# Performance work log

Measured on AMD Instinct MI355X. Metric: run time of the kernel, lower is better.

Reference implementation:

```python
import jax, jax.numpy as jnp
import numpy as np

N, F, H, K_SUB, DEPTH = 500_000, 64, 32, 16, 4
N_NODES = 2 ** DEPTH - 1   # 15 internal nodes
N_LEAVES = 2 ** DEPTH      # 16 leaves
SLOPE = 0.01               # torch LeakyReLU default negative_slope


def _leaky(v):
    return jnp.where(v >= 0, v, SLOPE * v)


def setup_inputs() -> dict:
    key = jax.random.key(0)
    ks = jax.random.split(key, 8)
    x = jax.random.normal(ks[0], (N, F), dtype=jnp.float32)
    subset_idx = jax.random.randint(ks[1], (N_NODES, K_SUB), 0, F, dtype=jnp.int32)
    W1 = jax.random.normal(ks[2], (N_NODES, H, K_SUB), dtype=jnp.float32) * (1.0 / np.sqrt(K_SUB))
    b1 = jnp.zeros((N_NODES, H), jnp.float32)
    W2 = jax.random.normal(ks[3], (N_NODES, H, H), dtype=jnp.float32) * (1.0 / np.sqrt(H))
    b2 = jnp.zeros((N_NODES, H), jnp.float32)
    W3 = jax.random.normal(ks[4], (N_NODES, 2, H), dtype=jnp.float32) * (1.0 / np.sqrt(H))
    b3 = jnp.zeros((N_NODES, 2), jnp.float32)
    # leaf 'best' constants (class modes precomputed by populate_best)
    leaf_best = jax.random.randint(ks[5], (N_LEAVES,), 0, 10).astype(jnp.float32)
    return {"x": x, "W1": W1, "b1": b1, "W2": W2, "b2": b2, "W3": W3, "b3": b3,
            "leaf_best": leaf_best, "subset_idx": subset_idx}


def _forward(x, W1, b1, W2, b2, W3, b3, leaf_best, subset_idx):
    n = x.shape[0]
    loc = jnp.zeros((n,), jnp.int32)   # local node index within current level
    off = 0
    for level in range(DEPTH):
        k = 2 ** level
        sl = slice(off, off + k)
        xs = x[:, subset_idx[sl]]                                   # [N, k, K_SUB]
        h = _leaky(jnp.einsum('nkf,khf->nkh', xs, W1[sl]) + b1[sl])  # [N, k, H]
        h = _leaky(jnp.einsum('nkh,kgh->nkg', h, W2[sl]) + b2[sl])   # [N, k, H]
        logits = jnp.einsum('nkh,koh->nko', h, W3[sl]) + b3[sl]      # [N, k, 2]
        p0 = jax.nn.softmax(logits, axis=-1)[..., 0]                 # [N, k]
        p0_row = jnp.take_along_axis(p0, loc[:, None], axis=1)[:, 0]
        bit = (p0_row < 0.5).astype(jnp.int32)  # 0 -> left, 1 -> right
        loc = 2 * loc + bit
        off += k
    return leaf_best[loc]  # [N]


def reference(x, W1, b1, W2, b2, W3, b3, leaf_best, subset_idx):
    return _forward(x, W1, b1, W2, b2, W3, b3, leaf_best, subset_idx)
```

## Files before the change

kernel.cpp:

```cpp
#include <hip/hip_runtime.h>

#define NF 64
#define NH 32
#define NK 16
#define NNODES 15
#define BLOCK 512
#define NWAVES (BLOCK / 64)


__global__ __attribute__((amdgpu_flat_work_group_size(BLOCK, BLOCK),
                          amdgpu_waves_per_eu(2, 4)))
void tree_mlp_kernel(
    const float* __restrict__ x,
    const float* __restrict__ W1, const float* __restrict__ b1,
    const float* __restrict__ W2, const float* __restrict__ b2,
    const float* __restrict__ W3, const float* __restrict__ b3,
    const float* __restrict__ leaf_best, const int* __restrict__ subset_idx,
    float* __restrict__ out, int N)
{
    __shared__ __align__(16) float W2Lv[8 * 1024];
    __shared__ int      subL[NNODES * NK];
    __shared__ unsigned permL[BLOCK];
    __shared__ int      sortL[64];

    const int tid  = threadIdx.x;
    const int lane = tid & 63;
    const int wv   = tid >> 6;

    for (int i = tid; i < NNODES * NK; i += BLOCK) subL[i] = subset_idx[i];
    {
        const float4* src = (const float4*)W2;
        float4* dst = (float4*)W2Lv;
        for (int i = tid; i < 256; i += BLOCK) dst[i] = src[i];
    }
    __syncthreads();

    const int s = blockIdx.x * BLOCK + tid;
    int valid = (s < N) ? 1 : 0;
    int id    = valid ? s : 0;
    int loc = 0, off = 0;

    #pragma unroll 1
    for (int level = 0; level < 4; ++level) {
        if (level > 0) {
            const int nb = 1 << level;
            int myrank = 0;
            #pragma unroll 1
            for (int b = 0; b < nb; ++b) {
                const unsigned long long m = __ballot(loc == b);
                if (loc == b)
                    myrank = __popcll(m & ((1ull << lane) - 1ull));
                if (lane == 0)
                    sortL[b * NWAVES + wv] = __popcll(m);
            }
            __syncthreads();

            {
                const int cnt4 = (1 << level) * 256;
                const float4* src = (const float4*)(W2 + (size_t)off * 1024);
                float4* dst = (float4*)W2Lv;
                for (int i = tid; i < cnt4; i += BLOCK) dst[i] = src[i];
            }
            if (wv == 0) {
                const int cnt = nb * NWAVES;
                int v = (lane < cnt) ? sortL[lane] : 0;
                int incl = v;
                #pragma unroll
                for (int d = 1; d < 64; d <<= 1) {
                    int t = __shfl_up(incl, d, 64);
                    if (lane >= d) incl += t;
                }
                if (lane < cnt) sortL[lane] = incl - v;
            }
            __syncthreads();

            const int slot = sortL[loc * NWAVES + wv] + myrank;
            permL[slot] = ((unsigned)id << 5) | ((unsigned)valid << 4) | (unsigned)loc;
            __syncthreads();
            const unsigned p = permL[tid];
            id    = (int)(p >> 5);
            valid = (int)((p >> 4) & 1u);
            loc   = (int)(p & 15u);
            __syncthreads();
        }

        const int node = off + loc;
        const float* xr = x + (size_t)id * NF;

        float xs[NK];
        const int* si = subL + node * NK;
        #pragma unroll
        for (int k = 0; k < NK; ++k) xs[k] = xr[si[k]];

        float h1v[NH];
        {
            const float4* w1g = (const float4*)(W1 + node * (NH * NK));
            const float*  b1g = b1 + node * NH;
            #pragma unroll
            for (int j = 0; j < NH; ++j) {
                float acc = b1g[j];
                #pragma unroll
                for (int q = 0; q < NK / 4; ++q) {
                    const float4 t = w1g[j * 4 + q];
                    acc += t.x * xs[q * 4 + 0];
                    acc += t.y * xs[q * 4 + 1];
                    acc += t.z * xs[q * 4 + 2];
                    acc += t.w * xs[q * 4 + 3];
                }
                h1v[j] = (acc >= 0.f) ? acc : 0.01f * acc;
            }
        }

        const float* w2l = W2Lv + (loc << 10);
        const float* bb2 = b2 + node * NH;
        const float* w3g = W3 + node * 2 * NH;
        float l0 = b3[node * 2 + 0];
        float l1 = b3[node * 2 + 1];

        #pragma unroll 2
        for (int g = 0; g < NH; ++g) {
            float acc = bb2[g];
            const float4* row = (const float4*)(w2l + g * NH);
            #pragma unroll
            for (int q = 0; q < NH / 4; ++q) {
                const float4 t = row[q];
                acc += t.x * h1v[q * 4 + 0];
                acc += t.y * h1v[q * 4 + 1];
                acc += t.z * h1v[q * 4 + 2];
                acc += t.w * h1v[q * 4 + 3];
            }
            const float h2 = (acc >= 0.f) ? acc : 0.01f * acc;
            l0 += w3g[g]      * h2;
            l1 += w3g[NH + g] * h2;
        }

        const int bit = (l0 < l1) ? 1 : 0;
        loc = 2 * loc + bit;
        off = 2 * off + 1;
    }

    if (valid) out[id] = leaf_best[loc];
}

extern "C" void kernel_launch(void* const* d_in, const int* in_sizes, int n_in,
                              void* d_out, int out_size, void* d_ws, size_t ws_size,
                              hipStream_t stream) {
    const float* x         = (const float*)d_in[0];
    const float* W1        = (const float*)d_in[1];
    const float* b1        = (const float*)d_in[2];
    const float* W2        = (const float*)d_in[3];
    const float* b2        = (const float*)d_in[4];
    const float* W3        = (const float*)d_in[5];
    const float* b3        = (const float*)d_in[6];
    const float* leaf_best = (const float*)d_in[7];
    const int*   subset    = (const int*)d_in[8];

    const int N = in_sizes[0] / NF;
    const int grid = (N + BLOCK - 1) / BLOCK;
    tree_mlp_kernel<<<grid, BLOCK, 0, stream>>>(
        x, W1, b1, W2, b2, W3, b3, leaf_best, subset, (float*)d_out, N);
}
```

Before: 487.1 us.

## Split tree traversal into per-level kernels with global bucketing by node

Replaces the single fused kernel, which re-sorts rows within each block at every level, with four launches. Each launch evaluates one tree level and scatters row ids into per-child global buckets using wave-level ballots and atomics. Every block then works on a single node, so weights are wave-uniform and read from global/scalar memory rather than staged in LDS. The cost is extra launches, a memset, gathered x reads through the id lists, and index traffic to a workspace buffer. The old fused kernel is kept as a fallback when the workspace is too small.

```diff
diff --git a/kernel.cpp b/kernel.cpp
--- a/kernel.cpp
+++ b/kernel.cpp
@@ -4,13 +4,147 @@
 #define NH 32
 #define NK 16
 #define NNODES 15
-#define BLOCK 512
-#define NWAVES (BLOCK / 64)
-
-
-__global__ __attribute__((amdgpu_flat_work_group_size(BLOCK, BLOCK),
+#define BLOCK 256
+#define MBLOCK 512
+#define MNWAVES (MBLOCK / 64)
+
+
+__device__ __forceinline__ int node_bit(
+    int id, int node,
+    const float* __restrict__ x,
+    const float* __restrict__ W1, const float* __restrict__ b1,
+    const float* __restrict__ W2, const float* __restrict__ b2,
+    const float* __restrict__ W3, const float* __restrict__ b3,
+    const int* __restrict__ subset_idx)
+{
+    const int* si = subset_idx + node * NK;
+    const float* xr = x + (size_t)id * NF;
+
+    float xs[NK];
+    #pragma unroll
+    for (int k = 0; k < NK; ++k) xs[k] = xr[si[k]];
+
+    int vnode = node;
+    asm volatile("" : "+v"(vnode));
+    float h1v[NH];
+    {
+        const float4* w1g = (const float4*)(W1 + (size_t)vnode * (NH * NK));
+        const float*  b1g = b1 + node * NH;
+        #pragma unroll
+        for (int j = 0; j < NH; ++j) {
+            float acc = b1g[j];
+            #pragma unroll
+            for (int q = 0; q < NK / 4; ++q) {
+                const float4 t = w1g[j * 4 + q];
+                acc += t.x * xs[q * 4 + 0];
+                acc += t.y * xs[q * 4 + 1];
+                acc += t.z * xs[q * 4 + 2];
+                acc += t.w * xs[q * 4 + 3];
+            }
+            h1v[j] = (acc >= 0.f) ? acc : 0.01f * acc;
+        }
+    }
+
+    const float* w2  = W2 + node * (NH * NH);
+    const float* bb2 = b2 + node * NH;
+    const float* w3  = W3 + node * 2 * NH;
+    float l0 = b3[node * 2 + 0];
+    float l1 = b3[node * 2 + 1];
+    #pragma unroll 2
+    for (int g = 0; g < NH; ++g) {
+        float acc = bb2[g];
+        #pragma unroll
+        for (int k = 0; k < NH; ++k) acc += w2[g * NH + k] * h1v[k];
+        const float h2 = (acc >= 0.f) ? acc : 0.01f * acc;
+        l0 += w3[g]      * h2;
+        l1 += w3[NH + g] * h2;
+    }
+    return (l0 < l1) ? 1 : 0;
+}
+
+__device__ __forceinline__ void scatter_pair(
+    int id, int valid, int bit, int c0, int c1, int N,
+    int* __restrict__ cnt, int* __restrict__ dst)
+{
+    const int lane = threadIdx.x & 63;
+    const unsigned long long lt = (lane == 0) ? 0ull : ((~0ull) >> (64 - lane));
+    const unsigned long long vm = __ballot(valid != 0);
+    const unsigned long long m1 = __ballot(valid && bit);
+    const unsigned long long m0 = vm & ~m1;
+    int b0 = 0, b1 = 0;
+    if (lane == 0) {
+        b0 = atomicAdd(&cnt[c0], __popcll(m0));
+        b1 = atomicAdd(&cnt[c1], __popcll(m1));
+    }
+    b0 = __shfl(b0, 0);
+    b1 = __shfl(b1, 0);
+    if (valid) {
+        const int  slot  = bit ? (b1 + __popcll(m1 & lt)) : (b0 + __popcll(m0 & lt));
+        const int  child = bit ? c1 : c0;
+        dst[(size_t)child * N + slot] = id;
+    }
+}
+
+__global__ void k_level0(
+    const float* __restrict__ x,
+    const float* __restrict__ W1, const float* __restrict__ b1,
+    const float* __restrict__ W2, const float* __restrict__ b2,
+    const float* __restrict__ W3, const float* __restrict__ b3,
+    const int* __restrict__ subset_idx,
+    int* __restrict__ cnt1, int* __restrict__ dst, int N)
+{
+    int id = blockIdx.x * BLOCK + threadIdx.x;
+    const int valid = (id < N) ? 1 : 0;
+    if (!valid) id = 0;
+    const int bit = node_bit(id, 0, x, W1, b1, W2, b2, W3, b3, subset_idx);
+    scatter_pair(id, valid, bit, 0, 1, N, cnt1, dst);
+}
+
+__global__ void k_level_mid(
+    const float* __restrict__ x,
+    const float* __restrict__ W1, const float* __restrict__ b1,
+    const float* __restrict__ W2, const float* __restrict__ b2,
+    const float* __restrict__ W3, const float* __restrict__ b3,
+    const int* __restrict__ subset_idx,
+    const int* __restrict__ cntIn, const int* __restrict__ src,
+    int* __restrict__ cntOut, int* __restrict__ dst,
+    int N, int CH, int off)
+{
+    const int n = blockIdx.x / CH;
+    const int c = blockIdx.x % CH;
+    const int cnt = cntIn[n];
+    if (c * BLOCK >= cnt) return;
+    const int i = c * BLOCK + (int)threadIdx.x;
+    const int valid = (i < cnt) ? 1 : 0;
+    const int id = src[(size_t)n * N + (valid ? i : 0)];
+    const int bit = node_bit(id, off + n, x, W1, b1, W2, b2, W3, b3, subset_idx);
+    scatter_pair(id, valid, bit, 2 * n, 2 * n + 1, N, cntOut, dst);
+}
+
+__global__ void k_level3(
+    const float* __restrict__ x,
+    const float* __restrict__ W1, const float* __restrict__ b1,
+    const float* __restrict__ W2, const float* __restrict__ b2,
+    const float* __restrict__ W3, const float* __restrict__ b3,
+    const int* __restrict__ subset_idx,
+    const int* __restrict__ cntIn, const int* __restrict__ src,
+    const float* __restrict__ leaf_best, float* __restrict__ out,
+    int N, int CH)
+{
+    const int n = blockIdx.x / CH;
+    const int c = blockIdx.x % CH;
+    const int cnt = cntIn[n];
+    if (c * BLOCK >= cnt) return;
+    const int i = c * BLOCK + (int)threadIdx.x;
+    if (i >= cnt) return;
+    const int id = src[(size_t)n * N + i];
+    const int bit = node_bit(id, 7 + n, x, W1, b1, W2, b2, W3, b3, subset_idx);
+    out[id] = leaf_best[2 * n + bit];
+}
+
+__global__ __attribute__((amdgpu_flat_work_group_size(MBLOCK, MBLOCK),
                           amdgpu_waves_per_eu(2, 4)))
-void tree_mlp_kernel(
+void tree_mlp_mono(
     const float* __restrict__ x,
     const float* __restrict__ W1, const float* __restrict__ b1,
     const float* __restrict__ W2, const float* __restrict__ b2,
@@ -20,22 +154,22 @@
 {
     __shared__ __align__(16) float W2Lv[8 * 1024];
     __shared__ int      subL[NNODES * NK];
-    __shared__ unsigned permL[BLOCK];
+    __shared__ unsigned permL[MBLOCK];
     __shared__ int      sortL[64];
 
     const int tid  = threadIdx.x;
     const int lane = tid & 63;
     const int wv   = tid >> 6;
 
-    for (int i = tid; i < NNODES * NK; i += BLOCK) subL[i] = subset_idx[i];
+    for (int i = tid; i < NNODES * NK; i += MBLOCK) subL[i] = subset_idx[i];
     {
-        const float4* src = (const float4*)W2;
-        float4* dst = (float4*)W2Lv;
-        for (int i = tid; i < 256; i += BLOCK) dst[i] = src[i];
+        const float4* srcp = (const float4*)W2;
+        float4* dstp = (float4*)W2Lv;
+        for (int i = tid; i < 256; i += MBLOCK) dstp[i] = srcp[i];
     }
     __syncthreads();
 
-    const int s = blockIdx.x * BLOCK + tid;
+    const int s = blockIdx.x * MBLOCK + tid;
     int valid = (s < N) ? 1 : 0;
     int id    = valid ? s : 0;
     int loc = 0, off = 0;
@@ -51,18 +185,17 @@
                 if (loc == b)
                     myrank = __popcll(m & ((1ull << lane) - 1ull));
                 if (lane == 0)
-                    sortL[b * NWAVES + wv] = __popcll(m);
+                    sortL[b * MNWAVES + wv] = __popcll(m);
             }
             __syncthreads();
-
             {
                 const int cnt4 = (1 << level) * 256;
-                const float4* src = (const float4*)(W2 + (size_t)off * 1024);
-                float4* dst = (float4*)W2Lv;
-                for (int i = tid; i < cnt4; i += BLOCK) dst[i] = src[i];
+                const float4* srcp = (const float4*)(W2 + (size_t)off * 1024);
+                float4* dstp = (float4*)W2Lv;
+                for (int i = tid; i < cnt4; i += MBLOCK) dstp[i] = srcp[i];
             }
             if (wv == 0) {
-                const int cnt = nb * NWAVES;
+                const int cnt = nb * MNWAVES;
                 int v = (lane < cnt) ? sortL[lane] : 0;
                 int incl = v;
                 #pragma unroll
@@ -73,8 +206,7 @@
                 if (lane < cnt) sortL[lane] = incl - v;
             }
             __syncthreads();
-
-            const int slot = sortL[loc * NWAVES + wv] + myrank;
+            const int slot = sortL[loc * MNWAVES + wv] + myrank;
             permL[slot] = ((unsigned)id << 5) | ((unsigned)valid << 4) | (unsigned)loc;
             __syncthreads();
             const unsigned p = permL[tid];
@@ -116,7 +248,6 @@
         const float* w3g = W3 + node * 2 * NH;
         float l0 = b3[node * 2 + 0];
         float l1 = b3[node * 2 + 1];
-
         #pragma unroll 2
         for (int g = 0; g < NH; ++g) {
             float acc = bb2[g];
@@ -156,7 +287,27 @@
     const int*   subset    = (const int*)d_in[8];
 
     const int N = in_sizes[0] / NF;
-    const int grid = (N + BLOCK - 1) / BLOCK;
-    tree_mlp_kernel<<<grid, BLOCK, 0, stream>>>(
-        x, W1, b1, W2, b2, W3, b3, leaf_best, subset, (float*)d_out, N);
-}
+
+    const size_t need = 256 + (size_t)12 * (size_t)N * sizeof(int);
+    if (ws_size >= need) {
+        int* cnt  = (int*)d_ws;
+        int* bufA = (int*)((char*)d_ws + 256);
+        int* bufB = bufA + (size_t)8 * N;
+        hipMemsetAsync(cnt, 0, 64, stream);
+
+        const int CH = (N + BLOCK - 1) / BLOCK;
+        k_level0<<<CH, BLOCK, 0, stream>>>(
+            x, W1, b1, W2, b2, W3, b3, subset, cnt + 0, bufA, N);
+        k_level_mid<<<2 * CH, BLOCK, 0, stream>>>(
+            x, W1, b1, W2, b2, W3, b3, subset, cnt + 0, bufA, cnt + 2, bufB, N, CH, 1);
+        k_level_mid<<<4 * CH, BLOCK, 0, stream>>>(
+            x, W1, b1, W2, b2, W3, b3, subset, cnt + 2, bufB, cnt + 6, bufA, N, CH, 3);
+        k_level3<<<8 * CH, BLOCK, 0, stream>>>(
+            x, W1, b1, W2, b2, W3, b3, subset, cnt + 6, bufA, leaf_best,
+            (float*)d_out, N, CH);
+    } else {
+        const int grid = (N + MBLOCK - 1) / MBLOCK;
+        tree_mlp_mono<<<grid, MBLOCK, 0, stream>>>(
+            x, W1, b1, W2, b2, W3, b3, leaf_best, subset, (float*)d_out, N);
+    }
+}
```

After: 928.8 us. +90.7%, slower.

## Process two samples per thread to reuse weight loads across samples

Applied to the files above, without the earlier changes.

Each thread now handles two samples (A and B), and each block covers twice as many rows. The per-level sort is extended so both samples get ranks, and after the sort each thread takes two adjacent slots, so a wave's 128 samples are mostly grouped by node. When every lane's two samples share a node, the W1, W2 (LDS) and W3 loads are reused for both samples' FMAs, halving weight-load traffic per sample. Otherwise a serial per-sample fallback runs. The trade-off is higher register pressure, with two sets of h1 arrays, which may lower occupancy.

```diff
diff --git a/kernel.cpp b/kernel.cpp
--- a/kernel.cpp
+++ b/kernel.cpp
@@ -6,6 +6,7 @@
 #define NNODES 15
 #define BLOCK 512
 #define NWAVES (BLOCK / 64)
+#define SPB (2 * BLOCK)
 
 
 __global__ __attribute__((amdgpu_flat_work_group_size(BLOCK, BLOCK),
@@ -20,12 +21,14 @@
 {
     __shared__ __align__(16) float W2Lv[8 * 1024];
     __shared__ int      subL[NNODES * NK];
-    __shared__ unsigned permL[BLOCK];
+    __shared__ unsigned permL[SPB];
     __shared__ int      sortL[64];
 
     const int tid  = threadIdx.x;
     const int lane = tid & 63;
     const int wv   = tid >> 6;
+    const unsigned long long lt =
+        (lane == 0) ? 0ull : ((~0ull) >> (64 - lane));
 
     for (int i = tid; i < NNODES * NK; i += BLOCK) subL[i] = subset_idx[i];
     {
@@ -35,23 +38,26 @@
     }
     __syncthreads();
 
-    const int s = blockIdx.x * BLOCK + tid;
-    int valid = (s < N) ? 1 : 0;
-    int id    = valid ? s : 0;
-    int loc = 0, off = 0;
+    const int base = blockIdx.x * SPB;
+    int idA = base + tid;
+    int idB = base + BLOCK + tid;
+    int vA = (idA < N) ? 1 : 0; if (!vA) idA = 0;
+    int vB = (idB < N) ? 1 : 0; if (!vB) idB = 0;
+    int locA = 0, locB = 0, off = 0;
 
     #pragma unroll 1
     for (int level = 0; level < 4; ++level) {
         if (level > 0) {
             const int nb = 1 << level;
-            int myrank = 0;
+            int rkA = 0, rkB = 0;
             #pragma unroll 1
             for (int b = 0; b < nb; ++b) {
-                const unsigned long long m = __ballot(loc == b);
-                if (loc == b)
-                    myrank = __popcll(m & ((1ull << lane) - 1ull));
+                const unsigned long long mA = __ballot(locA == b);
+                const unsigned long long mB = __ballot(locB == b);
+                if (locA == b) rkA = __popcll(mA & lt);
+                if (locB == b) rkB = __popcll(mA) + __popcll(mB & lt);
                 if (lane == 0)
-                    sortL[b * NWAVES + wv] = __popcll(m);
+                    sortL[b * NWAVES + wv] = __popcll(mA) + __popcll(mB);
             }
             __syncthreads();
 
@@ -74,72 +80,146 @@
             }
             __syncthreads();
 
-            const int slot = sortL[loc * NWAVES + wv] + myrank;
-            permL[slot] = ((unsigned)id << 5) | ((unsigned)valid << 4) | (unsigned)loc;
-            __syncthreads();
-            const unsigned p = permL[tid];
-            id    = (int)(p >> 5);
-            valid = (int)((p >> 4) & 1u);
-            loc   = (int)(p & 15u);
+            const int slotA = sortL[locA * NWAVES + wv] + rkA;
+            const int slotB = sortL[locB * NWAVES + wv] + rkB;
+            permL[slotA] = ((unsigned)idA << 5) | ((unsigned)vA << 4) | (unsigned)locA;
+            permL[slotB] = ((unsigned)idB << 5) | ((unsigned)vB << 4) | (unsigned)locB;
+            __syncthreads();
+            const unsigned pA = permL[wv * 128 + 2 * lane];
+            const unsigned pB = permL[wv * 128 + 2 * lane + 1];
+            idA = (int)(pA >> 5); vA = (int)((pA >> 4) & 1u); locA = (int)(pA & 15u);
+            idB = (int)(pB >> 5); vB = (int)((pB >> 4) & 1u); locB = (int)(pB & 15u);
             __syncthreads();
         }
 
-        const int node = off + loc;
-        const float* xr = x + (size_t)id * NF;
-
-        float xs[NK];
-        const int* si = subL + node * NK;
-        #pragma unroll
-        for (int k = 0; k < NK; ++k) xs[k] = xr[si[k]];
-
-        float h1v[NH];
-        {
-            const float4* w1g = (const float4*)(W1 + node * (NH * NK));
-            const float*  b1g = b1 + node * NH;
+        const int nodeA = off + locA;
+        const int nodeB = off + locB;
+        int bitA, bitB;
+
+        if (__all(nodeA == nodeB)) {
+            const int* si = subL + nodeA * NK;
+            const float* xrA = x + (size_t)idA * NF;
+            const float* xrB = x + (size_t)idB * NF;
+            float xsA[NK], xsB[NK];
             #pragma unroll
-            for (int j = 0; j < NH; ++j) {
-                float acc = b1g[j];
-                #pragma unroll
-                for (int q = 0; q < NK / 4; ++q) {
-                    const float4 t = w1g[j * 4 + q];
-                    acc += t.x * xs[q * 4 + 0];
-                    acc += t.y * xs[q * 4 + 1];
-                    acc += t.z * xs[q * 4 + 2];
-                    acc += t.w * xs[q * 4 + 3];
-                }
-                h1v[j] = (acc >= 0.f) ? acc : 0.01f * acc;
+            for (int k = 0; k < NK; ++k) {
+                const int f = si[k];
+                xsA[k] = xrA[f];
+                xsB[k] = xrB[f];
+            }
+
+            float h1A[NH], h1B[NH];
+            {
+                const float4* w1g = (const float4*)(W1 + nodeA * (NH * NK));
+                const float*  b1g = b1 + nodeA * NH;
+                #pragma unroll
+                for (int j = 0; j < NH; ++j) {
+                    const float bj = b1g[j];
+                    float aA = bj, aB = bj;
+                    #pragma unroll
+                    for (int q = 0; q < NK / 4; ++q) {
+                        const float4 t = w1g[j * 4 + q];
+                        aA += t.x * xsA[q * 4 + 0]; aB += t.x * xsB[q * 4 + 0];
+                        aA += t.y * xsA[q * 4 + 1]; aB += t.y * xsB[q * 4 + 1];
+                        aA += t.z * xsA[q * 4 + 2]; aB += t.z * xsB[q * 4 + 2];
+                        aA += t.w * xsA[q * 4 + 3]; aB += t.w * xsB[q * 4 + 3];
+                    }
+                    h1A[j] = (aA >= 0.f) ? aA : 0.01f * aA;
+                    h1B[j] = (aB >= 0.f) ? aB : 0.01f * aB;
+                }
+            }
+
+            const float* w2l = W2Lv + (locA << 10);
+            const float* bb2 = b2 + nodeA * NH;
+            const float* w3g = W3 + nodeA * 2 * NH;
+            const float bi0 = b3[nodeA * 2 + 0];
+            const float bi1 = b3[nodeA * 2 + 1];
+            float l0A = bi0, l1A = bi1, l0B = bi0, l1B = bi1;
+
+            #pragma unroll 2
+            for (int g = 0; g < NH; ++g) {
+                const float bg = bb2[g];
+                float aA = bg, aB = bg;
+                const float4* row = (const float4*)(w2l + g * NH);
+                #pragma unroll
+                for (int q = 0; q < NH / 4; ++q) {
+                    const float4 t = row[q];
+                    aA += t.x * h1A[q * 4 + 0]; aB += t.x * h1B[q * 4 + 0];
+                    aA += t.y * h1A[q * 4 + 1]; aB += t.y * h1B[q * 4 + 1];
+                    aA += t.z * h1A[q * 4 + 2]; aB += t.z * h1B[q * 4 + 2];
+                    aA += t.w * h1A[q * 4 + 3]; aB += t.w * h1B[q * 4 + 3];
+                }
+                const float h2A = (aA >= 0.f) ? aA : 0.01f * aA;
+                const float h2B = (aB >= 0.f) ? aB : 0.01f * aB;
+                const float wa = w3g[g];
+                const float wb = w3g[NH + g];
+                l0A += wa * h2A; l1A += wb * h2A;
+                l0B += wa * h2B; l1B += wb * h2B;
+            }
+            bitA = (l0A < l1A) ? 1 : 0;
+            bitB = (l0B < l1B) ? 1 : 0;
+        } else {
+            #pragma unroll 1
+            for (int s2 = 0; s2 < 2; ++s2) {
+                const int idS  = s2 ? idB : idA;
+                const int locS = s2 ? locB : locA;
+                const int node = off + locS;
+                const int* si = subL + node * NK;
+                const float* xr = x + (size_t)idS * NF;
+                float xs[NK];
+                #pragma unroll
+                for (int k = 0; k < NK; ++k) xs[k] = xr[si[k]];
+
+                float h1v[NH];
+                const float4* w1g = (const float4*)(W1 + node * (NH * NK));
+                const float*  b1g = b1 + node * NH;
+                #pragma unroll
+                for (int j = 0; j < NH; ++j) {
+                    float acc = b1g[j];
+                    #pragma unroll
+                    for (int q = 0; q < NK / 4; ++q) {
+                        const float4 t = w1g[j * 4 + q];
+                        acc += t.x * xs[q * 4 + 0];
+                        acc += t.y * xs[q * 4 + 1];
+                        acc += t.z * xs[q * 4 + 2];
+                        acc += t.w * xs[q * 4 + 3];
+                    }
+                    h1v[j] = (acc >= 0.f) ? acc : 0.01f * acc;
+                }
+
+                const float* w2l = W2Lv + (locS << 10);
+                const float* bb2 = b2 + node * NH;
+                const float* w3g = W3 + node * 2 * NH;
+                float l0 = b3[node * 2 + 0];
+                float l1 = b3[node * 2 + 1];
+                #pragma unroll 2
+                for (int g = 0; g < NH; ++g) {
+                    float acc = bb2[g];
+                    const float4* row = (const float4*)(w2l + g * NH);
+                    #pragma unroll
+                    for (int q = 0; q < NH / 4; ++q) {
+                        const float4 t = row[q];
+                        acc += t.x * h1v[q * 4 + 0];
+                        acc += t.y * h1v[q * 4 + 1];
+                        acc += t.z * h1v[q * 4 + 2];
+                        acc += t.w * h1v[q * 4 + 3];
+                    }
+                    const float h2 = (acc >= 0.f) ? acc : 0.01f * acc;
+                    l0 += w3g[g]      * h2;
+                    l1 += w3g[NH + g] * h2;
+                }
+                const int bit = (l0 < l1) ? 1 : 0;
+                if (s2) bitB = bit; else bitA = bit;
             }
         }
 
-        const float* w2l = W2Lv + (loc << 10);
-        const float* bb2 = b2 + node * NH;
-        const float* w3g = W3 + node * 2 * NH;
-        float l0 = b3[node * 2 + 0];
-        float l1 = b3[node * 2 + 1];
-
-        #pragma unroll 2
-        for (int g = 0; g < NH; ++g) {
-            float acc = bb2[g];
-            const float4* row = (const float4*)(w2l + g * NH);
-            #pragma unroll
-            for (int q = 0; q < NH / 4; ++q) {
-                const float4 t = row[q];
-                acc += t.x * h1v[q * 4 + 0];
-                acc += t.y * h1v[q * 4 + 1];
-                acc += t.z * h1v[q * 4 + 2];
-                acc += t.w * h1v[q * 4 + 3];
-            }
-            const float h2 = (acc >= 0.f) ? acc : 0.01f * acc;
-            l0 += w3g[g]      * h2;
-            l1 += w3g[NH + g] * h2;
-        }
-
-        const int bit = (l0 < l1) ? 1 : 0;
-        loc = 2 * loc + bit;
+        locA = 2 * locA + bitA;
+        locB = 2 * locB + bitB;
         off = 2 * off + 1;
     }
 
-    if (valid) out[id] = leaf_best[loc];
+    if (vA) out[idA] = leaf_best[locA];
+    if (vB) out[idB] = leaf_best[locB];
 }
 
 extern "C" void kernel_launch(void* const* d_in, const int* in_sizes, int n_in,
@@ -156,7 +236,7 @@
     const int*   subset    = (const int*)d_in[8];
 
     const int N = in_sizes[0] / NF;
-    const int grid = (N + BLOCK - 1) / BLOCK;
+    const int grid = (N + SPB - 1) / SPB;
     tree_mlp_kernel<<<grid, BLOCK, 0, stream>>>(
         x, W1, b1, W2, b2, W3, b3, leaf_best, subset, (float*)d_out, N);
 }
```

Measured after the change: 434.3 us. -10.8%, faster.
